# Kernel tuning notes

Hardware: AMD Instinct MI355X
Metric: run time of the kernel (lower is better)

Reference implementation:

```python
import jax, jax.numpy as jnp
import numpy as np

NUM_EXPERTS = 64
D_MODEL = 1024
N_TOKENS = 4096
TOP_K = 2
CAPACITY = 512


def setup_inputs() -> dict:
    key = jax.random.key(0)
    k1, k2, k3 = jax.random.split(key, 3)
    x = jax.random.normal(k1, (N_TOKENS, D_MODEL), dtype=jnp.float32)
    gate_w = 0.02 * jax.random.normal(k2, (NUM_EXPERTS, D_MODEL), dtype=jnp.float32)
    expert_w = 0.02 * jax.random.normal(k3, (NUM_EXPERTS, D_MODEL, D_MODEL), dtype=jnp.float32)
    return {"x": x, "gate_w": gate_w, "expert_w": expert_w}


def reference(x, gate_w, expert_w):
    N, d = x.shape
    E = gate_w.shape[0]
    # --- gating: top-2 + softmax over the two selected logits ---
    logits = x @ gate_w.T                         # [N, E]
    top_logits, top_idx = jax.lax.top_k(logits, TOP_K)
    weights = jax.nn.softmax(top_logits, axis=-1) # [N, 2]
    flat_idx = top_idx.reshape(-1)                # [2N], expert per token-slot
    flat_w = weights.reshape(-1)                  # [2N]
    tokens = jnp.repeat(x, TOP_K, axis=0)         # [2N, d] (repeat_interleave)
    # --- dispatch: stable sort by expert, position within expert ---
    order = jnp.argsort(flat_idx)                 # stable
    se = flat_idx[order]                          # sorted expert ids
    starts = jnp.searchsorted(se, jnp.arange(E))  # first row of each expert
    pos = jnp.arange(se.shape[0]) - starts[se]    # slot within expert
    buf = jnp.zeros((E, CAPACITY, d), x.dtype).at[se, pos].set(tokens[order], mode="drop")
    # --- per-expert GEMM (Linear no bias: y = x @ W.T) ---
    eout = jnp.einsum("ecd,efd->ecf", buf, expert_w)  # [E, C, d]
    # --- combine: gather back, scale by gate weight, unsort, sum top-2 ---
    out_sorted = eout[se, jnp.clip(pos, 0, CAPACITY - 1)] * flat_w[order][:, None]
    combined = jnp.zeros_like(tokens).at[order].set(out_sorted)
    return combined.reshape(N, TOP_K, d).sum(axis=1)
```

## Files before the change

### kernel.cpp

```cpp
#include <hip/hip_runtime.h>
#include <stdint.h>

#define N_TOKENS 4096
#define D_MODEL  1024
#define NUM_EXP  64
#define CAP      512
#define KSLICES  8

typedef unsigned short u16;
typedef __bf16 bf16x8 __attribute__((ext_vector_type(8)));
typedef float  f32x4  __attribute__((ext_vector_type(4)));
typedef const __attribute__((address_space(1))) void* as1cvp;
typedef __attribute__((address_space(3))) void*       as3vp;

__device__ __forceinline__ uint32_t f2bf_bits(float f) {
  union { float f; uint32_t u; } c; c.f = f;
  uint32_t u = c.u;
  u += 0x7fffu + ((u >> 16) & 1u);
  return u >> 16;
}

__global__ __launch_bounds__(256) void gate_partial_kernel(
    const float* __restrict__ x, const float* __restrict__ gw,
    float* __restrict__ part, u16* __restrict__ xb)
{
  const int ks  = blockIdx.x;
  const int m0  = blockIdx.y * 64;
  const int tid = threadIdx.x;
  const int ty = tid >> 4, tx = tid & 15;
  __shared__ float4 As[64][16];
  __shared__ float4 Bs[64][16];
  float acc[4][4] = {};
  for (int kt = 0; kt < 2; ++kt) {
    const int k0 = ks * 128 + kt * 64;
    __syncthreads();
    #pragma unroll
    for (int i = 0; i < 4; ++i) {
      int idx = tid + i * 256;
      int r = idx >> 4, c = idx & 15;
      float4 v = *(const float4*)&x[(size_t)(m0 + r) * D_MODEL + k0 + c * 4];
      As[r][c ^ (r >> 2)] = v;
      uint32_t lo = f2bf_bits(v.x) | (f2bf_bits(v.y) << 16);
      uint32_t hi = f2bf_bits(v.z) | (f2bf_bits(v.w) << 16);
      *(uint2*)&xb[(size_t)(m0 + r) * D_MODEL + k0 + c * 4] = make_uint2(lo, hi);
      float4 w = *(const float4*)&gw[(size_t)r * D_MODEL + k0 + c * 4];
      Bs[r][c ^ (r >> 2)] = w;
    }
    __syncthreads();
    #pragma unroll
    for (int kk = 0; kk < 16; ++kk) {
      float4 a[4], b[4];
      #pragma unroll
      for (int j = 0; j < 4; ++j) a[j] = As[ty * 4 + j][kk ^ ty];
      #pragma unroll
      for (int j = 0; j < 4; ++j) b[j] = Bs[tx * 4 + j][kk ^ tx];
      #pragma unroll
      for (int j = 0; j < 4; ++j)
        #pragma unroll
        for (int i2 = 0; i2 < 4; ++i2) {
          acc[j][i2] += a[j].x * b[i2].x;
          acc[j][i2] += a[j].y * b[i2].y;
          acc[j][i2] += a[j].z * b[i2].z;
          acc[j][i2] += a[j].w * b[i2].w;
        }
    }
  }
  #pragma unroll
  for (int j = 0; j < 4; ++j) {
    float4 o = make_float4(acc[j][0], acc[j][1], acc[j][2], acc[j][3]);
    size_t t = (size_t)m0 + ty * 4 + j;
    *(float4*)&part[((size_t)ks * N_TOKENS + t) * NUM_EXP + tx * 4] = o;
  }
}

__global__ __launch_bounds__(256) void topk_dispatch_kernel(
    const float* __restrict__ part, int* __restrict__ cnt,
    int* __restrict__ tok, float* __restrict__ wts, int* __restrict__ dst)
{
  const int t = blockIdx.x * 256 + threadIdx.x;
  float l[64];
  const float4* p4 = (const float4*)part;
  #pragma unroll
  for (int c = 0; c < 16; ++c) {
    float4 v = p4[(size_t)t * 16 + c];
    l[c*4+0] = v.x; l[c*4+1] = v.y; l[c*4+2] = v.z; l[c*4+3] = v.w;
  }
  #pragma unroll
  for (int s = 1; s < KSLICES; ++s) {
    #pragma unroll
    for (int c = 0; c < 16; ++c) {
      float4 v = p4[((size_t)s * N_TOKENS + t) * 16 + c];
      l[c*4+0] += v.x; l[c*4+1] += v.y; l[c*4+2] += v.z; l[c*4+3] += v.w;
    }
  }
  float b1 = -3.4e38f; int e1 = 0;
  #pragma unroll
  for (int e = 0; e < 64; ++e) { if (l[e] > b1) { b1 = l[e]; e1 = e; } }
  float b2 = -3.4e38f; int e2 = 0;
  #pragma unroll
  for (int e = 0; e < 64; ++e) { if (e != e1 && l[e] > b2) { b2 = l[e]; e2 = e; } }
  float ex = expf(b2 - b1);
  float w1 = 1.0f / (1.0f + ex);
  float w2 = ex   / (1.0f + ex);
  int p = atomicAdd(&cnt[e1], 1);
  if (p < CAP) { tok[e1*CAP+p] = t; wts[e1*CAP+p] = w1; dst[e1*CAP+p] = 2*t; }
  p = atomicAdd(&cnt[e2], 1);
  if (p < CAP) { tok[e2*CAP+p] = t; wts[e2*CAP+p] = w2; dst[e2*CAP+p] = 2*t+1; }
}

__global__ __launch_bounds__(512) void expert_gemm_kernel(
    const u16* __restrict__ xb, const float* __restrict__ ew,
    const int* __restrict__ cnt, const int* __restrict__ tok,
    const float* __restrict__ wts, const int* __restrict__ dst,
    float* __restrict__ ybuf)
{
  const int e = blockIdx.z;
  int ne = cnt[e]; ne = ne > CAP ? CAP : ne;
  const int m0 = blockIdx.y * 256;
  if (m0 >= ne) return;
  const int n0 = blockIdx.x * 128;
  const int tid = threadIdx.x;
  const int wid = tid >> 6, lane = tid & 63;
  const int wm = wid & 3, wn = wid >> 2;

  __shared__ u16  Alds[256 * 64];
  __shared__ u16  Blds[128 * 64];
  __shared__ int   tokL[256];
  __shared__ float wL[256];
  __shared__ int   dL[256];

  if (tid < 256) {
    int g = m0 + tid;
    bool v = g < ne;
    tokL[tid] = v ? tok[e * CAP + g] : 0;
    wL[tid]   = v ? wts[e * CAP + g] : 0.f;
    dL[tid]   = v ? dst[e * CAP + g] : 0;
  }
  __syncthreads();

  const u16* asrc[4];
  #pragma unroll
  for (int i = 0; i < 4; ++i) {
    int idx = tid + i * 512;
    int r = idx >> 3, c = idx & 7;
    int cs = c ^ (r & 7);
    asrc[i] = xb + (size_t)tokL[r] * D_MODEL + cs * 8;
  }
  const float* Wb = ew + (size_t)e * D_MODEL * D_MODEL + (size_t)n0 * D_MODEL;

  f32x4 acc[4][4] = {};

  for (int k0 = 0; k0 < D_MODEL; k0 += 64) {
    __syncthreads();
    #pragma unroll
    for (int i = 0; i < 4; ++i)
      __builtin_amdgcn_global_load_lds((as1cvp)(asrc[i] + k0),
                                       (as3vp)(Alds + (tid + i * 512) * 8), 16, 0, 0);
    #pragma unroll
    for (int i = 0; i < 4; ++i) {
      int idx = tid + i * 512;
      int r = idx >> 4, c = idx & 15;
      float4 v = *(const float4*)&Wb[(size_t)r * D_MODEL + k0 + c * 4];
      uint32_t lo = f2bf_bits(v.x) | (f2bf_bits(v.y) << 16);
      uint32_t hi = f2bf_bits(v.z) | (f2bf_bits(v.w) << 16);
      int boff = r * 128 + (((c >> 1) ^ (r & 7)) << 4) + (c & 1) * 8;
      *(uint2*)((char*)Blds + boff) = make_uint2(lo, hi);
    }
    __syncthreads();
    #pragma unroll
    for (int kk = 0; kk < 2; ++kk) {
      const int kbyte = kk * 64 + (lane >> 4) * 16;
      bf16x8 a[4], b[4];
      #pragma unroll
      for (int mi = 0; mi < 4; ++mi) {
        int r = wm * 64 + mi * 16 + (lane & 15);
        a[mi] = *(const bf16x8*)((const char*)Alds + r * 128 + (kbyte ^ ((r & 7) << 4)));
      }
      #pragma unroll
      for (int nj = 0; nj < 4; ++nj) {
        int r = wn * 64 + nj * 16 + (lane & 15);
        b[nj] = *(const bf16x8*)((const char*)Blds + r * 128 + (kbyte ^ ((r & 7) << 4)));
      }
      #pragma unroll
      for (int mi = 0; mi < 4; ++mi)
        #pragma unroll
        for (int nj = 0; nj < 4; ++nj)
          acc[mi][nj] = __builtin_amdgcn_mfma_f32_16x16x32_bf16(a[mi], b[nj], acc[mi][nj], 0, 0, 0);
    }
  }

  #pragma unroll
  for (int mi = 0; mi < 4; ++mi) {
    #pragma unroll
    for (int r4 = 0; r4 < 4; ++r4) {
      int rl = wm * 64 + mi * 16 + (lane >> 4) * 4 + r4;
      if (m0 + rl < ne) {
        float wg = wL[rl];
        size_t dbase = (size_t)dL[rl] * D_MODEL + n0 + wn * 64 + (lane & 15);
        #pragma unroll
        for (int nj = 0; nj < 4; ++nj)
          ybuf[dbase + nj * 16] = acc[mi][nj][r4] * wg;
      }
    }
  }
}

__global__ __launch_bounds__(256) void combine_kernel(
    const float* __restrict__ ybuf, float* __restrict__ out)
{
  size_t i = (size_t)blockIdx.x * 256 + threadIdx.x;
  size_t t = i >> 8, c = i & 255;
  const float4* a4 = (const float4*)(ybuf + (2 * t) * D_MODEL);
  const float4* b4 = (const float4*)(ybuf + (2 * t + 1) * D_MODEL);
  float4 a = a4[c], b = b4[c];
  float4 o; o.x = a.x + b.x; o.y = a.y + b.y; o.z = a.z + b.z; o.w = a.w + b.w;
  ((float4*)out)[i] = o;
}

extern "C" void kernel_launch(void* const* d_in, const int* in_sizes, int n_in,
                              void* d_out, int out_size, void* d_ws, size_t ws_size,
                              hipStream_t stream) {
  const float* x  = (const float*)d_in[0];
  const float* gw = (const float*)d_in[1];
  const float* ew = (const float*)d_in[2];
  float* out = (float*)d_out;
  char* ws = (char*)d_ws;
  int*   cnt  = (int*)(ws + 0);
  int*   tok  = (int*)(ws + 1024);
  float* wts  = (float*)(ws + 132096);
  int*   dst  = (int*)(ws + 263168);
  float* part = (float*)(ws + 394240);
  u16*   xb   = (u16*)  (ws + 8782848);
  float* ybuf = (float*)(ws + 17171456);

  hipMemsetAsync(cnt, 0, 64 * sizeof(int), stream);
  gate_partial_kernel<<<dim3(KSLICES, 64), 256, 0, stream>>>(x, gw, part, xb);
  topk_dispatch_kernel<<<16, 256, 0, stream>>>(part, cnt, tok, wts, dst);
  expert_gemm_kernel<<<dim3(8, 2, 64), 512, 0, stream>>>(xb, ew, cnt, tok, wts, dst, ybuf);
  combine_kernel<<<4096, 256, 0, stream>>>(ybuf, out);
}
```

Baseline: 468.6 us.

## Fuse gating with top-k, double-buffer expert GEMM, atomically combine into output

Gating GEMM and top-2 selection are merged into one kernel that writes dispatch lists directly, removing the partial-logit buffer and the separate top-k launch. The expert GEMM tile shrinks to 128x128 with twice as many M blocks. It gains double-buffered LDS with prefetch of the next K slice, overlapping global loads with MFMA. The combine kernel and intermediate ybuf are replaced by float atomic adds into a zeroed output, at the cost of an extra memset, atomic traffic and nondeterministic summation order. Each expert weight tile is now streamed by more blocks, which raises weight reads.

```diff
diff --git a/kernel.cpp b/kernel.cpp
--- a/kernel.cpp
+++ b/kernel.cpp
@@ -5,7 +5,6 @@
 #define D_MODEL  1024
 #define NUM_EXP  64
 #define CAP      512
-#define KSLICES  8
 
 typedef unsigned short u16;
 typedef __bf16 bf16x8 __attribute__((ext_vector_type(8)));
@@ -20,173 +19,185 @@
   return u >> 16;
 }
 
-__global__ __launch_bounds__(256) void gate_partial_kernel(
+__global__ __launch_bounds__(256) void gate_fused_kernel(
     const float* __restrict__ x, const float* __restrict__ gw,
-    float* __restrict__ part, u16* __restrict__ xb)
+    u16* __restrict__ xb, int* __restrict__ cnt,
+    int* __restrict__ tok, float* __restrict__ wts)
 {
-  const int ks  = blockIdx.x;
-  const int m0  = blockIdx.y * 64;
+  const int t0  = blockIdx.x * 16;
   const int tid = threadIdx.x;
-  const int ty = tid >> 4, tx = tid & 15;
-  __shared__ float4 As[64][16];
-  __shared__ float4 Bs[64][16];
-  float acc[4][4] = {};
-  for (int kt = 0; kt < 2; ++kt) {
-    const int k0 = ks * 128 + kt * 64;
+  const int tt = tid >> 4, eg = tid & 15;
+
+  __shared__ float4 xs[16][32];
+  __shared__ float4 gws[64][32];
+  __shared__ float  lg[16][64];
+
+  float acc[4] = {0.f, 0.f, 0.f, 0.f};
+
+  for (int kc = 0; kc < 8; ++kc) {
+    const int k0 = kc * 128;
     __syncthreads();
     #pragma unroll
-    for (int i = 0; i < 4; ++i) {
+    for (int i = 0; i < 2; ++i) {
       int idx = tid + i * 256;
-      int r = idx >> 4, c = idx & 15;
-      float4 v = *(const float4*)&x[(size_t)(m0 + r) * D_MODEL + k0 + c * 4];
-      As[r][c ^ (r >> 2)] = v;
+      int r = idx >> 5, c = idx & 31;
+      float4 v = *(const float4*)&x[(size_t)(t0 + r) * D_MODEL + k0 + c * 4];
+      xs[r][c ^ r] = v;
       uint32_t lo = f2bf_bits(v.x) | (f2bf_bits(v.y) << 16);
       uint32_t hi = f2bf_bits(v.z) | (f2bf_bits(v.w) << 16);
-      *(uint2*)&xb[(size_t)(m0 + r) * D_MODEL + k0 + c * 4] = make_uint2(lo, hi);
-      float4 w = *(const float4*)&gw[(size_t)r * D_MODEL + k0 + c * 4];
-      Bs[r][c ^ (r >> 2)] = w;
+      *(uint2*)&xb[(size_t)(t0 + r) * D_MODEL + k0 + c * 4] = make_uint2(lo, hi);
+    }
+    #pragma unroll
+    for (int i = 0; i < 8; ++i) {
+      int idx = tid + i * 256;
+      int r = idx >> 5, c = idx & 31;
+      gws[r][c ^ (r & 31)] = *(const float4*)&gw[(size_t)r * D_MODEL + k0 + c * 4];
     }
     __syncthreads();
     #pragma unroll
-    for (int kk = 0; kk < 16; ++kk) {
-      float4 a[4], b[4];
-      #pragma unroll
-      for (int j = 0; j < 4; ++j) a[j] = As[ty * 4 + j][kk ^ ty];
-      #pragma unroll
-      for (int j = 0; j < 4; ++j) b[j] = Bs[tx * 4 + j][kk ^ tx];
-      #pragma unroll
-      for (int j = 0; j < 4; ++j)
-        #pragma unroll
-        for (int i2 = 0; i2 < 4; ++i2) {
-          acc[j][i2] += a[j].x * b[i2].x;
-          acc[j][i2] += a[j].y * b[i2].y;
-          acc[j][i2] += a[j].z * b[i2].z;
-          acc[j][i2] += a[j].w * b[i2].w;
-        }
-    }
-  }
-  #pragma unroll
-  for (int j = 0; j < 4; ++j) {
-    float4 o = make_float4(acc[j][0], acc[j][1], acc[j][2], acc[j][3]);
-    size_t t = (size_t)m0 + ty * 4 + j;
-    *(float4*)&part[((size_t)ks * N_TOKENS + t) * NUM_EXP + tx * 4] = o;
-  }
-}
-
-__global__ __launch_bounds__(256) void topk_dispatch_kernel(
-    const float* __restrict__ part, int* __restrict__ cnt,
-    int* __restrict__ tok, float* __restrict__ wts, int* __restrict__ dst)
-{
-  const int t = blockIdx.x * 256 + threadIdx.x;
-  float l[64];
-  const float4* p4 = (const float4*)part;
-  #pragma unroll
-  for (int c = 0; c < 16; ++c) {
-    float4 v = p4[(size_t)t * 16 + c];
-    l[c*4+0] = v.x; l[c*4+1] = v.y; l[c*4+2] = v.z; l[c*4+3] = v.w;
-  }
-  #pragma unroll
-  for (int s = 1; s < KSLICES; ++s) {
-    #pragma unroll
-    for (int c = 0; c < 16; ++c) {
-      float4 v = p4[((size_t)s * N_TOKENS + t) * 16 + c];
-      l[c*4+0] += v.x; l[c*4+1] += v.y; l[c*4+2] += v.z; l[c*4+3] += v.w;
-    }
-  }
-  float b1 = -3.4e38f; int e1 = 0;
-  #pragma unroll
-  for (int e = 0; e < 64; ++e) { if (l[e] > b1) { b1 = l[e]; e1 = e; } }
-  float b2 = -3.4e38f; int e2 = 0;
-  #pragma unroll
-  for (int e = 0; e < 64; ++e) { if (e != e1 && l[e] > b2) { b2 = l[e]; e2 = e; } }
-  float ex = expf(b2 - b1);
-  float w1 = 1.0f / (1.0f + ex);
-  float w2 = ex   / (1.0f + ex);
-  int p = atomicAdd(&cnt[e1], 1);
-  if (p < CAP) { tok[e1*CAP+p] = t; wts[e1*CAP+p] = w1; dst[e1*CAP+p] = 2*t; }
-  p = atomicAdd(&cnt[e2], 1);
-  if (p < CAP) { tok[e2*CAP+p] = t; wts[e2*CAP+p] = w2; dst[e2*CAP+p] = 2*t+1; }
+    for (int c = 0; c < 32; ++c) {
+      float4 xa = xs[tt][c ^ tt];
+      #pragma unroll
+      for (int j = 0; j < 4; ++j) {
+        int e = eg * 4 + j;
+        float4 wv = gws[e][c ^ (e & 31)];
+        acc[j] += xa.x * wv.x; acc[j] += xa.y * wv.y;
+        acc[j] += xa.z * wv.z; acc[j] += xa.w * wv.w;
+      }
+    }
+  }
+  #pragma unroll
+  for (int j = 0; j < 4; ++j) lg[tt][eg * 4 + j] = acc[j];
+  __syncthreads();
+
+  if (tid < 16) {
+    float b1 = -3.4e38f; int e1 = 0;
+    #pragma unroll
+    for (int e = 0; e < 64; ++e) { float v = lg[tid][e]; if (v > b1) { b1 = v; e1 = e; } }
+    float b2 = -3.4e38f; int e2 = 0;
+    #pragma unroll
+    for (int e = 0; e < 64; ++e) { float v = lg[tid][e]; if (e != e1 && v > b2) { b2 = v; e2 = e; } }
+    float ex = expf(b2 - b1);
+    float w1 = 1.0f / (1.0f + ex);
+    float w2 = ex   / (1.0f + ex);
+    int t = t0 + tid;
+    int p = atomicAdd(&cnt[e1], 1);
+    if (p < CAP) { tok[e1 * CAP + p] = t; wts[e1 * CAP + p] = w1; }
+    p = atomicAdd(&cnt[e2], 1);
+    if (p < CAP) { tok[e2 * CAP + p] = t; wts[e2 * CAP + p] = w2; }
+  }
 }
 
 __global__ __launch_bounds__(512) void expert_gemm_kernel(
     const u16* __restrict__ xb, const float* __restrict__ ew,
     const int* __restrict__ cnt, const int* __restrict__ tok,
-    const float* __restrict__ wts, const int* __restrict__ dst,
-    float* __restrict__ ybuf)
+    const float* __restrict__ wts, float* __restrict__ out)
 {
   const int e = blockIdx.z;
   int ne = cnt[e]; ne = ne > CAP ? CAP : ne;
-  const int m0 = blockIdx.y * 256;
+  const int m0 = blockIdx.y * 128;
   if (m0 >= ne) return;
   const int n0 = blockIdx.x * 128;
   const int tid = threadIdx.x;
   const int wid = tid >> 6, lane = tid & 63;
-  const int wm = wid & 3, wn = wid >> 2;
-
-  __shared__ u16  Alds[256 * 64];
-  __shared__ u16  Blds[128 * 64];
-  __shared__ int   tokL[256];
-  __shared__ float wL[256];
-  __shared__ int   dL[256];
-
-  if (tid < 256) {
+  const int wm = wid & 1, wn = wid >> 1;
+
+  __shared__ u16  Alds[2][128 * 64];
+  __shared__ u16  Blds[2][128 * 64];
+  __shared__ int   tokL[128];
+  __shared__ float wL[128];
+
+  if (tid < 128) {
     int g = m0 + tid;
     bool v = g < ne;
     tokL[tid] = v ? tok[e * CAP + g] : 0;
     wL[tid]   = v ? wts[e * CAP + g] : 0.f;
-    dL[tid]   = v ? dst[e * CAP + g] : 0;
   }
   __syncthreads();
 
-  const u16* asrc[4];
+  const u16* asrc[2];
+  #pragma unroll
+  for (int i = 0; i < 2; ++i) {
+    int idx = tid + i * 512;
+    int r = idx >> 3, c = idx & 7;
+    asrc[i] = xb + (size_t)tokL[r] * D_MODEL + (c ^ (r & 7)) * 8;
+  }
+  const float* Wb = ew + (size_t)e * D_MODEL * D_MODEL + (size_t)n0 * D_MODEL;
+  const float* bsrc[4]; int boff[4];
   #pragma unroll
   for (int i = 0; i < 4; ++i) {
     int idx = tid + i * 512;
-    int r = idx >> 3, c = idx & 7;
-    int cs = c ^ (r & 7);
-    asrc[i] = xb + (size_t)tokL[r] * D_MODEL + cs * 8;
-  }
-  const float* Wb = ew + (size_t)e * D_MODEL * D_MODEL + (size_t)n0 * D_MODEL;
-
-  f32x4 acc[4][4] = {};
-
-  for (int k0 = 0; k0 < D_MODEL; k0 += 64) {
-    __syncthreads();
-    #pragma unroll
-    for (int i = 0; i < 4; ++i)
-      __builtin_amdgcn_global_load_lds((as1cvp)(asrc[i] + k0),
-                                       (as3vp)(Alds + (tid + i * 512) * 8), 16, 0, 0);
+    int r = idx >> 4, c = idx & 15;
+    bsrc[i] = Wb + (size_t)r * D_MODEL + c * 4;
+    boff[i] = r * 128 + (((c >> 1) ^ (r & 7)) << 4) + (c & 1) * 8;
+  }
+
+  #pragma unroll
+  for (int i = 0; i < 2; ++i)
+    __builtin_amdgcn_global_load_lds((as1cvp)(asrc[i]),
+                                     (as3vp)((char*)&Alds[0][0] + (tid + i * 512) * 16), 16, 0, 0);
+  {
+    float4 bv[4];
+    #pragma unroll
+    for (int i = 0; i < 4; ++i) bv[i] = *(const float4*)(bsrc[i]);
     #pragma unroll
     for (int i = 0; i < 4; ++i) {
-      int idx = tid + i * 512;
-      int r = idx >> 4, c = idx & 15;
-      float4 v = *(const float4*)&Wb[(size_t)r * D_MODEL + k0 + c * 4];
-      uint32_t lo = f2bf_bits(v.x) | (f2bf_bits(v.y) << 16);
-      uint32_t hi = f2bf_bits(v.z) | (f2bf_bits(v.w) << 16);
-      int boff = r * 128 + (((c >> 1) ^ (r & 7)) << 4) + (c & 1) * 8;
-      *(uint2*)((char*)Blds + boff) = make_uint2(lo, hi);
-    }
-    __syncthreads();
+      uint32_t lo = f2bf_bits(bv[i].x) | (f2bf_bits(bv[i].y) << 16);
+      uint32_t hi = f2bf_bits(bv[i].z) | (f2bf_bits(bv[i].w) << 16);
+      *(uint2*)((char*)&Blds[0][0] + boff[i]) = make_uint2(lo, hi);
+    }
+  }
+  __syncthreads();
+
+  f32x4 acc[4][2] = {};
+
+  for (int t = 0; t < 16; ++t) {
+    const char* ldsA = (const char*)&Alds[t & 1][0];
+    const char* ldsB = (const char*)&Blds[t & 1][0];
+    char* ldsAn = (char*)&Alds[(t & 1) ^ 1][0];
+    char* ldsBn = (char*)&Blds[(t & 1) ^ 1][0];
+
+    float4 bv[4];
+    if (t < 15) {
+      const int kn = (t + 1) * 64;
+      #pragma unroll
+      for (int i = 0; i < 2; ++i)
+        __builtin_amdgcn_global_load_lds((as1cvp)(asrc[i] + kn),
+                                         (as3vp)(ldsAn + (tid + i * 512) * 16), 16, 0, 0);
+      #pragma unroll
+      for (int i = 0; i < 4; ++i) bv[i] = *(const float4*)(bsrc[i] + kn);
+    }
+
     #pragma unroll
     for (int kk = 0; kk < 2; ++kk) {
       const int kbyte = kk * 64 + (lane >> 4) * 16;
-      bf16x8 a[4], b[4];
+      bf16x8 a[4], b[2];
       #pragma unroll
       for (int mi = 0; mi < 4; ++mi) {
         int r = wm * 64 + mi * 16 + (lane & 15);
-        a[mi] = *(const bf16x8*)((const char*)Alds + r * 128 + (kbyte ^ ((r & 7) << 4)));
-      }
-      #pragma unroll
-      for (int nj = 0; nj < 4; ++nj) {
-        int r = wn * 64 + nj * 16 + (lane & 15);
-        b[nj] = *(const bf16x8*)((const char*)Blds + r * 128 + (kbyte ^ ((r & 7) << 4)));
+        a[mi] = *(const bf16x8*)(ldsA + r * 128 + (kbyte ^ ((r & 7) << 4)));
+      }
+      #pragma unroll
+      for (int nj = 0; nj < 2; ++nj) {
+        int r = wn * 32 + nj * 16 + (lane & 15);
+        b[nj] = *(const bf16x8*)(ldsB + r * 128 + (kbyte ^ ((r & 7) << 4)));
       }
       #pragma unroll
       for (int mi = 0; mi < 4; ++mi)
         #pragma unroll
-        for (int nj = 0; nj < 4; ++nj)
+        for (int nj = 0; nj < 2; ++nj)
           acc[mi][nj] = __builtin_amdgcn_mfma_f32_16x16x32_bf16(a[mi], b[nj], acc[mi][nj], 0, 0, 0);
     }
+
+    if (t < 15) {
+      #pragma unroll
+      for (int i = 0; i < 4; ++i) {
+        uint32_t lo = f2bf_bits(bv[i].x) | (f2bf_bits(bv[i].y) << 16);
+        uint32_t hi = f2bf_bits(bv[i].z) | (f2bf_bits(bv[i].w) << 16);
+        *(uint2*)(ldsBn + boff[i]) = make_uint2(lo, hi);
+      }
+    }
+    __syncthreads();
   }
 
   #pragma unroll
@@ -196,25 +207,13 @@
       int rl = wm * 64 + mi * 16 + (lane >> 4) * 4 + r4;
       if (m0 + rl < ne) {
         float wg = wL[rl];
-        size_t dbase = (size_t)dL[rl] * D_MODEL + n0 + wn * 64 + (lane & 15);
+        size_t dbase = (size_t)tokL[rl] * D_MODEL + n0 + wn * 32 + (lane & 15);
         #pragma unroll
-        for (int nj = 0; nj < 4; ++nj)
-          ybuf[dbase + nj * 16] = acc[mi][nj][r4] * wg;
-      }
-    }
-  }
-}
-
-__global__ __launch_bounds__(256) void combine_kernel(
-    const float* __restrict__ ybuf, float* __restrict__ out)
-{
-  size_t i = (size_t)blockIdx.x * 256 + threadIdx.x;
-  size_t t = i >> 8, c = i & 255;
-  const float4* a4 = (const float4*)(ybuf + (2 * t) * D_MODEL);
-  const float4* b4 = (const float4*)(ybuf + (2 * t + 1) * D_MODEL);
-  float4 a = a4[c], b = b4[c];
-  float4 o; o.x = a.x + b.x; o.y = a.y + b.y; o.z = a.z + b.z; o.w = a.w + b.w;
-  ((float4*)out)[i] = o;
+        for (int nj = 0; nj < 2; ++nj)
+          unsafeAtomicAdd(&out[dbase + nj * 16], acc[mi][nj][r4] * wg);
+      }
+    }
+  }
 }
 
 extern "C" void kernel_launch(void* const* d_in, const int* in_sizes, int n_in,
@@ -225,17 +224,13 @@
   const float* ew = (const float*)d_in[2];
   float* out = (float*)d_out;
   char* ws = (char*)d_ws;
-  int*   cnt  = (int*)(ws + 0);
-  int*   tok  = (int*)(ws + 1024);
-  float* wts  = (float*)(ws + 132096);
-  int*   dst  = (int*)(ws + 263168);
-  float* part = (float*)(ws + 394240);
-  u16*   xb   = (u16*)  (ws + 8782848);
-  float* ybuf = (float*)(ws + 17171456);
+  int*   cnt = (int*)(ws + 0);
+  int*   tok = (int*)(ws + 1024);
+  float* wts = (float*)(ws + 132096);
+  u16*   xb  = (u16*)  (ws + 263168);
 
   hipMemsetAsync(cnt, 0, 64 * sizeof(int), stream);
-  gate_partial_kernel<<<dim3(KSLICES, 64), 256, 0, stream>>>(x, gw, part, xb);
-  topk_dispatch_kernel<<<16, 256, 0, stream>>>(part, cnt, tok, wts, dst);
-  expert_gemm_kernel<<<dim3(8, 2, 64), 512, 0, stream>>>(xb, ew, cnt, tok, wts, dst, ybuf);
-  combine_kernel<<<4096, 256, 0, stream>>>(ybuf, out);
-}
+  hipMemsetAsync(out, 0, (size_t)N_TOKENS * D_MODEL * sizeof(float), stream);
+  gate_fused_kernel<<<256, 256, 0, stream>>>(x, gw, xb, cnt, tok, wts);
+  expert_gemm_kernel<<<dim3(8, 4, 64), 512, 0, stream>>>(xb, ew, cnt, tok, wts, out);
+}
```

Result: slower. 535.6 us (+14.3%).
